# Kernel optimization log

Hardware: AMD Instinct MI355X
Metric: run time of the kernel (lower is better)

The kernel has to match this reference:

```python
import jax, jax.numpy as jnp
import numpy as np

DT = 0.1
TAU_MIN = 1.0
TAU_MAX = 10.0
LN_EPS = 1e-5


def setup_inputs() -> dict:
    key = jax.random.key(0)
    ks = jax.random.split(key, 8)
    B, S, I, H = 64, 1024, 256, 512
    s_in = 1.0 / np.sqrt(I)
    s_rec = 1.0 / np.sqrt(H)
    s_tau1 = 1.0 / np.sqrt(I + H)
    s_tau2 = 1.0 / np.sqrt(H)
    return {
        "x": jax.random.normal(ks[0], (B, S, I), dtype=jnp.float32),
        "h0": jnp.zeros((B, H), dtype=jnp.float32),
        "W_in": jax.random.uniform(ks[1], (H, I), jnp.float32, -s_in, s_in),
        "b_in": jax.random.uniform(ks[2], (H,), jnp.float32, -s_in, s_in),
        "W_rec": jax.random.uniform(ks[3], (H, H), jnp.float32, -s_rec, s_rec),
        "tau_w1": jax.random.uniform(ks[4], (H, I + H), jnp.float32, -s_tau1, s_tau1),
        "tau_b1": jax.random.uniform(ks[5], (H,), jnp.float32, -s_tau1, s_tau1),
        "tau_w2": jax.random.uniform(ks[6], (1, H), jnp.float32, -s_tau2, s_tau2),
        "tau_b2": jax.random.uniform(ks[7], (1,), jnp.float32, -s_tau2, s_tau2),
        "gamma": jnp.ones((H,), dtype=jnp.float32),
        "beta": jnp.zeros((H,), dtype=jnp.float32),
    }


def _layernorm(h, gamma, beta):
    mu = jnp.mean(h, axis=-1, keepdims=True)
    var = jnp.mean(jnp.square(h - mu), axis=-1, keepdims=True)
    return (h - mu) * jax.lax.rsqrt(var + LN_EPS) * gamma + beta


def reference(x, h0, W_in, b_in, W_rec, tau_w1, tau_b1, tau_w2, tau_b2, gamma, beta):
    # x: [B, S, I] -> scan over time with carry h: [B, H]
    def step(h, x_t):
        combined = jnp.concatenate([x_t, h], axis=-1)                     # [B, I+H]
        t_hid = jnp.tanh(combined @ tau_w1.T + tau_b1)                    # [B, H]
        tau_raw = jax.nn.sigmoid(t_hid @ tau_w2.T + tau_b2)               # [B, 1]
        tau = TAU_MIN + (TAU_MAX - TAU_MIN) * tau_raw                     # [B, 1]
        f_xh = jnp.tanh(x_t @ W_in.T + b_in + h @ W_rec.T)                # [B, H]
        h_new = h + DT * (-h + f_xh) / tau
        h_new = _layernorm(h_new, gamma, beta)
        return h_new, (h_new, tau)

    xs = jnp.swapaxes(x, 0, 1)                                            # [S, B, I]
    h_final, (outs, taus) = jax.lax.scan(step, h0, xs)
    output = jnp.swapaxes(outs, 0, 1)                                     # [B, S, H]
    tau_history = jnp.swapaxes(taus, 0, 1)                                # [B, S, 1]
    return output, h_final, tau_history
```

## Files before the change

### kernel.cpp

```cpp
#include <hip/hip_runtime.h>

#define S_LEN 1024
#define BATCH 64
#define I_DIM 256
#define H_DIM 512
#define NCL 8
#define NRK 8
#define ROWS 8
#define FPW 64
#define HSTR 520
#define XSTR 264
#define POLL_CAP 16384

typedef short short8 __attribute__((ext_vector_type(8)));
typedef float floatx4 __attribute__((ext_vector_type(4)));
typedef unsigned short ushortx4 __attribute__((ext_vector_type(4)));

__device__ inline unsigned short f2bf(float x){
  unsigned u = __float_as_uint(x);
  u += 0x7fffu + ((u >> 16) & 1u);
  return (unsigned short)(u >> 16);
}
__device__ inline float bf2f(unsigned short s){
  return __uint_as_float(((unsigned)s) << 16);
}
__device__ inline float fast_tanh(float x){
  float e = __expf(2.0f * x);
  return 1.0f - 2.0f / (e + 1.0f);
}
__device__ inline float fast_sigmoid(float x){
  return 1.0f / (1.0f + __expf(-x));
}
__device__ inline short8 cvt8(const float* p){
  short8 r;
#pragma unroll
  for (int j = 0; j < 8; j++) r[j] = (short)f2bf(p[j]);
  return r;
}

__global__ __launch_bounds__(256) void convert_weights_kernel(
  const float* __restrict__ W_in, const float* __restrict__ tau_w1,
  unsigned short* __restrict__ Wbf, unsigned short* __restrict__ Tbf)
{
  const int f = blockIdx.x, k = threadIdx.x;
  Wbf[f * I_DIM + k] = f2bf(W_in[(size_t)f * I_DIM + k]);
  Tbf[f * I_DIM + k] = f2bf(tau_w1[(size_t)f * (I_DIM + H_DIM) + k]);
}

__global__ __launch_bounds__(256) void precompute_kernel(
  const float* __restrict__ x, const unsigned short* __restrict__ Wbf,
  const unsigned short* __restrict__ Tbf,
  const float* __restrict__ b_in, const float* __restrict__ tau_b1,
  unsigned short* __restrict__ A_in, unsigned short* __restrict__ A_tau)
{
  __shared__ unsigned short xs[BATCH * XSTR];
  const int t = blockIdx.x, tid = threadIdx.x;
  {
    const int br = tid >> 2, pp = tid & 3;
    const float* xrow = x + ((size_t)br * S_LEN + t) * I_DIM + pp * 64;
    unsigned short* drow = xs + br * XSTR + pp * 64;
#pragma unroll
    for (int c = 0; c < 16; c++){
      float4 v = *(const float4*)(xrow + c * 4);
      ushortx4 o; o[0] = f2bf(v.x); o[1] = f2bf(v.y); o[2] = f2bf(v.z); o[3] = f2bf(v.w);
      *(ushortx4*)(drow + c * 4) = o;
    }
  }
  __syncthreads();

  const int w = tid >> 6, l15 = tid & 15, q = (tid & 63) >> 4;
#pragma unroll 1
  for (int fb = 0; fb < 8; fb++){
    const int F = fb * 64 + w * 16 + l15;
    floatx4 accf[4], acct[4];
#pragma unroll
    for (int m = 0; m < 4; m++){ accf[m] = (floatx4){0,0,0,0}; acct[m] = (floatx4){0,0,0,0}; }
#pragma unroll
    for (int kc = 0; kc < 8; kc++){
      const int k0 = kc * 32 + q * 8;
      short8 bw = *(const short8*)&Wbf[F * I_DIM + k0];
      short8 bt = *(const short8*)&Tbf[F * I_DIM + k0];
#pragma unroll
      for (int m = 0; m < 4; m++){
        short8 a = *(const short8*)&xs[(m * 16 + l15) * XSTR + k0];
        accf[m] = __builtin_amdgcn_mfma_f32_16x16x32_bf16(a, bw, accf[m], 0, 0, 0);
        acct[m] = __builtin_amdgcn_mfma_f32_16x16x32_bf16(a, bt, acct[m], 0, 0, 0);
      }
    }
    const float bi = b_in[F], bt1 = tau_b1[F];
#pragma unroll
    for (int m = 0; m < 4; m++){
      ushortx4 pf, pt;
#pragma unroll
      for (int i2 = 0; i2 < 4; i2++){ pf[i2] = f2bf(accf[m][i2] + bi); pt[i2] = f2bf(acct[m][i2] + bt1); }
      const size_t base = ((size_t)t * H_DIM + F) * BATCH + m * 16 + q * 4;
      *(ushortx4*)(A_in + base) = pf;
      *(ushortx4*)(A_tau + base) = pt;
    }
  }
}

__global__ __launch_bounds__(256, 1) void scan_kernel(
  const float* __restrict__ h0, const float* __restrict__ W_rec,
  const float* __restrict__ tau_w1, const float* __restrict__ tau_w2,
  const float* __restrict__ tau_b2_p, const float* __restrict__ gamma,
  const float* __restrict__ beta,
  const unsigned short* __restrict__ A_in, const unsigned short* __restrict__ A_tau,
  unsigned short* __restrict__ bc_f, float* __restrict__ bc_td,
  unsigned int* __restrict__ flags,
  float* __restrict__ out0, float* __restrict__ outh, float* __restrict__ outtau)
{
  __shared__ unsigned short hB[16 * HSTR];

  const int tid = threadIdx.x;
  const int cl   = blockIdx.x & (NCL - 1);
  const int rank = blockIdx.x >> 3;

  for (int idx = tid; idx < 16 * HSTR; idx += 256) hB[idx] = 0;

  const int w = tid >> 6, l64 = tid & 63, l15 = tid & 15, q = (tid & 63) >> 4;
  const int fl = l15;
  const int rb0 = (l64 >> 4) * 4;
  const bool pvalid = (l64 < 32);
  const int F0 = rank * FPW + w * 16;
  const int Fl = F0 + l15;
  const int rr = tid >> 5;
  const int cc = tid & 31;

  short8 wr[16], wt[16];
#pragma unroll
  for (int kc = 0; kc < 16; kc++){
    const int k = kc * 32 + q * 8;
    wr[kc] = cvt8(&W_rec[(size_t)Fl * H_DIM + k]);
    wt[kc] = cvt8(&tau_w1[(size_t)Fl * (I_DIM + H_DIM) + I_DIM + k]);
  }
  const float tw2v = tau_w2[Fl];
  const float tb2 = tau_b2_p[0];
  __syncthreads();

  float h_reg[16], gamr[16], betr[16];
  {
    const int b = cl * ROWS + rr;
#pragma unroll
    for (int j = 0; j < 16; j++){
      float hv = h0[(size_t)b * H_DIM + cc * 16 + j];
      h_reg[j] = hv;
      hB[rr * HSTR + cc * 16 + j] = f2bf(hv);
      gamr[j] = gamma[cc * 16 + j];
      betr[j] = beta[cc * 16 + j];
    }
  }

  ushortx4 afr = (ushortx4){0,0,0,0}, atr = (ushortx4){0,0,0,0};
  if (pvalid){
    const size_t aidx = ((size_t)Fl) * BATCH + cl * ROWS + rb0;
    afr = *(const ushortx4*)&A_in[aidx];
    atr = *(const ushortx4*)&A_tau[aidx];
  }
  __syncthreads();

  for (int t = 0; t < S_LEN; t++){
    const int par = t & 1;

    floatx4 af = {0,0,0,0}, at4 = {0,0,0,0};
#pragma unroll
    for (int kc = 0; kc < 16; kc++){
      short8 ha = *(const short8*)&hB[l15 * HSTR + kc * 32 + q * 8];
      af  = __builtin_amdgcn_mfma_f32_16x16x32_bf16(ha, wr[kc], af,  0, 0, 0);
      at4 = __builtin_amdgcn_mfma_f32_16x16x32_bf16(ha, wt[kc], at4, 0, 0, 0);
    }

    unsigned short* bcF = bc_f + ((size_t)(par * NCL + cl) * ROWS) * H_DIM;
    float pd[4];
#pragma unroll
    for (int i2 = 0; i2 < 4; i2++){
      float vf = fast_tanh(af[i2]  + bf2f(afr[i2]));
      float vt = fast_tanh(at4[i2] + bf2f(atr[i2]));
      pd[i2] = vt * tw2v;
      unsigned pv = (unsigned)f2bf(vf);
      unsigned ov = (unsigned)__shfl_xor((int)pv, 1);
      if (pvalid && !(fl & 1)){
        unsigned short* p = bcF + (size_t)(rb0 + i2) * H_DIM + F0 + fl;
        __hip_atomic_store((unsigned*)p, pv | (ov << 16),
                           __ATOMIC_RELAXED, __HIP_MEMORY_SCOPE_AGENT);
      }
    }
#pragma unroll
    for (int i2 = 0; i2 < 4; i2++){
      pd[i2] += __shfl_xor(pd[i2], 1);
      pd[i2] += __shfl_xor(pd[i2], 2);
      pd[i2] += __shfl_xor(pd[i2], 4);
      pd[i2] += __shfl_xor(pd[i2], 8);
    }
    if (pvalid && fl == 0){
      float* p = bc_td + ((size_t)(par * NCL + cl) * 32 + rank * 4 + w) * ROWS + rb0;
#pragma unroll
      for (int i2 = 0; i2 < 4; i2++)
        __hip_atomic_store(p + i2, pd[i2], __ATOMIC_RELAXED, __HIP_MEMORY_SCOPE_AGENT);
    }

    __builtin_amdgcn_s_waitcnt(0);
    __syncthreads();
    if (tid == 0)
      __hip_atomic_store(&flags[cl * NRK + rank], (unsigned)(t + 1),
                         __ATOMIC_RELAXED, __HIP_MEMORY_SCOPE_AGENT);
    if (t + 1 < S_LEN && pvalid){
      const size_t aidx = ((size_t)(t + 1) * H_DIM + Fl) * BATCH + cl * ROWS + rb0;
      afr = *(const ushortx4*)&A_in[aidx];
      atr = *(const ushortx4*)&A_tau[aidx];
    }
    if (w == 0 && l64 < NRK){
      const unsigned tgt = (unsigned)(t + 1);
      const unsigned int* fp = &flags[cl * NRK + l64];
      int guard = 0;
      while (__hip_atomic_load(fp, __ATOMIC_RELAXED, __HIP_MEMORY_SCOPE_AGENT) < tgt){
        if (++guard > POLL_CAP) break;
        __builtin_amdgcn_s_sleep(1);
      }
    }
    asm volatile("" ::: "memory");
    __syncthreads();

    const unsigned long long* p64 = (const unsigned long long*)
      (bc_f + (((size_t)(par * NCL + cl) * ROWS) + rr) * H_DIM + cc * 16);
    const float* tdp = bc_td + ((size_t)(par * NCL + cl) * 32 + cc) * ROWS + rr;
    unsigned long long v0 = __hip_atomic_load(p64 + 0, __ATOMIC_RELAXED, __HIP_MEMORY_SCOPE_AGENT);
    unsigned long long v1 = __hip_atomic_load(p64 + 1, __ATOMIC_RELAXED, __HIP_MEMORY_SCOPE_AGENT);
    unsigned long long v2 = __hip_atomic_load(p64 + 2, __ATOMIC_RELAXED, __HIP_MEMORY_SCOPE_AGENT);
    unsigned long long v3 = __hip_atomic_load(p64 + 3, __ATOMIC_RELAXED, __HIP_MEMORY_SCOPE_AGENT);
    float td = __hip_atomic_load(tdp, __ATOMIC_RELAXED, __HIP_MEMORY_SCOPE_AGENT);

    td += __shfl_xor(td, 1); td += __shfl_xor(td, 2);
    td += __shfl_xor(td, 4); td += __shfl_xor(td, 8);
    td += __shfl_xor(td, 16);
    const float tau = 1.0f + 9.0f * fast_sigmoid(td + tb2);
    const float c2 = 0.1f / tau, c1 = 1.0f - c2;

    float fv[16];
#pragma unroll
    for (int e = 0; e < 4; e++){
      fv[e]      = bf2f((unsigned short)(v0 >> (16 * e)));
      fv[4 + e]  = bf2f((unsigned short)(v1 >> (16 * e)));
      fv[8 + e]  = bf2f((unsigned short)(v2 >> (16 * e)));
      fv[12 + e] = bf2f((unsigned short)(v3 >> (16 * e)));
    }
    float hp[16]; float s1 = 0.f, s2 = 0.f;
#pragma unroll
    for (int j = 0; j < 16; j++){
      float v = c1 * h_reg[j] + c2 * fv[j];
      hp[j] = v; s1 += v; s2 += v * v;
    }
    s1 += __shfl_xor(s1, 1);  s2 += __shfl_xor(s2, 1);
    s1 += __shfl_xor(s1, 2);  s2 += __shfl_xor(s2, 2);
    s1 += __shfl_xor(s1, 4);  s2 += __shfl_xor(s2, 4);
    s1 += __shfl_xor(s1, 8);  s2 += __shfl_xor(s2, 8);
    s1 += __shfl_xor(s1, 16); s2 += __shfl_xor(s2, 16);
    const float mu = s1 * (1.0f / 512.0f);
    const float var = s2 * (1.0f / 512.0f) - mu * mu;
    const float rs = rsqrtf(var + 1e-5f);
#pragma unroll
    for (int j = 0; j < 16; j++) h_reg[j] = (hp[j] - mu) * rs * gamr[j] + betr[j];

#pragma unroll
    for (int u = 0; u < 2; u++){
      short8 hv;
#pragma unroll
      for (int e = 0; e < 8; e++) hv[e] = (short)f2bf(h_reg[u * 8 + e]);
      *(short8*)&hB[rr * HSTR + cc * 16 + u * 8] = hv;
    }

    if (rr == rank){
      float* dst = out0 + ((size_t)(cl * ROWS + rr) * S_LEN + t) * H_DIM + cc * 16;
#pragma unroll
      for (int j = 0; j < 16; j++) dst[j] = h_reg[j];
      if (cc == 0) outtau[(size_t)(cl * ROWS + rr) * S_LEN + t] = tau;
      if (t == S_LEN - 1){
        float* dh = outh + (size_t)(cl * ROWS + rr) * H_DIM + cc * 16;
#pragma unroll
        for (int j = 0; j < 16; j++) dh[j] = h_reg[j];
      }
    }
    __syncthreads();
  }
}

extern "C" void kernel_launch(void* const* d_in, const int* in_sizes, int n_in,
                              void* d_out, int out_size, void* d_ws, size_t ws_size,
                              hipStream_t stream) {
  const float* x      = (const float*)d_in[0];
  const float* h0     = (const float*)d_in[1];
  const float* W_in   = (const float*)d_in[2];
  const float* b_in   = (const float*)d_in[3];
  const float* W_rec  = (const float*)d_in[4];
  const float* tau_w1 = (const float*)d_in[5];
  const float* tau_b1 = (const float*)d_in[6];
  const float* tau_w2 = (const float*)d_in[7];
  const float* tau_b2 = (const float*)d_in[8];
  const float* gamma  = (const float*)d_in[9];
  const float* beta   = (const float*)d_in[10];

  char* ws = (char*)d_ws;
  unsigned short* A_in   = (unsigned short*)(ws);
  unsigned short* A_tau  = (unsigned short*)(ws + 67108864);
  unsigned short* bc_f   = (unsigned short*)(ws + 134217728);
  float*          bc_td  = (float*)(ws + 134348800);
  unsigned int*   flags  = (unsigned int*)(ws + 134365184);
  unsigned short* Wbf    = (unsigned short*)(ws + 134366208);
  unsigned short* Tbf    = (unsigned short*)(ws + 134628352);

  float* out0   = (float*)d_out;
  float* outh   = out0 + (size_t)BATCH * S_LEN * H_DIM;
  float* outtau = outh + (size_t)BATCH * H_DIM;

  hipMemsetAsync(flags, 0, 1024, stream);
  convert_weights_kernel<<<dim3(H_DIM), 256, 0, stream>>>(W_in, tau_w1, Wbf, Tbf);
  precompute_kernel<<<dim3(S_LEN), 256, 0, stream>>>(x, Wbf, Tbf, b_in, tau_b1, A_in, A_tau);
  scan_kernel<<<dim3(NCL * NRK), 256, 0, stream>>>(h0, W_rec, tau_w1, tau_w2, tau_b2, gamma, beta,
                                                   A_in, A_tau, bc_f, bc_td, flags,
                                                   out0, outh, outtau);
}
```

Baseline: 4.368 ms.

## Map each scan cluster to one XCD and use workgroup-scope atomics for exchange

At startup, each block reads its hardware XCD id and takes a slot in a per-XCD counter. This lets it join a cluster whose 8 ranks all sit on the same XCD. When every XCD holds a multiple of 8 blocks and a trial handshake succeeds, per-step communication uses workgroup-scope atomics, which are meant to stay in the local L2 and avoid device-coherent traffic. The flags are also padded to 64-byte spacing to avoid false sharing. This adds startup handshakes and falls back to agent scope otherwise, but relying on workgroup scope for cross-block visibility goes beyond what the memory model guarantees.

```diff
diff --git a/kernel.cpp b/kernel.cpp
--- a/kernel.cpp
+++ b/kernel.cpp
@@ -11,6 +11,8 @@
 #define HSTR 520
 #define XSTR 264
 #define POLL_CAP 16384
+#define HSHAKE_CAP 200000
+#define TRIAL_CAP 30000
 
 typedef short short8 __attribute__((ext_vector_type(8)));
 typedef float floatx4 __attribute__((ext_vector_type(4)));
@@ -36,6 +38,27 @@
 #pragma unroll
   for (int j = 0; j < 8; j++) r[j] = (short)f2bf(p[j]);
   return r;
+}
+
+__device__ inline void comm_st_u32(unsigned* p, unsigned v, bool fast){
+  if (fast) __hip_atomic_store(p, v, __ATOMIC_RELAXED, __HIP_MEMORY_SCOPE_WORKGROUP);
+  else      __hip_atomic_store(p, v, __ATOMIC_RELAXED, __HIP_MEMORY_SCOPE_AGENT);
+}
+__device__ inline void comm_st_f32(float* p, float v, bool fast){
+  if (fast) __hip_atomic_store(p, v, __ATOMIC_RELAXED, __HIP_MEMORY_SCOPE_WORKGROUP);
+  else      __hip_atomic_store(p, v, __ATOMIC_RELAXED, __HIP_MEMORY_SCOPE_AGENT);
+}
+__device__ inline unsigned comm_ld_u32(unsigned* p, bool fast){
+  if (fast) return __hip_atomic_fetch_add(p, 0u, __ATOMIC_RELAXED, __HIP_MEMORY_SCOPE_WORKGROUP);
+  else      return __hip_atomic_load(p, __ATOMIC_RELAXED, __HIP_MEMORY_SCOPE_AGENT);
+}
+__device__ inline unsigned long long comm_ld_u64(unsigned long long* p, bool fast){
+  if (fast) return __hip_atomic_fetch_add(p, 0ull, __ATOMIC_RELAXED, __HIP_MEMORY_SCOPE_WORKGROUP);
+  else      return __hip_atomic_load(p, __ATOMIC_RELAXED, __HIP_MEMORY_SCOPE_AGENT);
+}
+__device__ inline float comm_ld_f32(float* p, bool fast){
+  if (fast) return __hip_atomic_fetch_add(p, 0.0f, __ATOMIC_RELAXED, __HIP_MEMORY_SCOPE_WORKGROUP);
+  else      return __hip_atomic_load(p, __ATOMIC_RELAXED, __HIP_MEMORY_SCOPE_AGENT);
 }
 
 __global__ __launch_bounds__(256) void convert_weights_kernel(
@@ -111,12 +134,77 @@
   float* __restrict__ out0, float* __restrict__ outh, float* __restrict__ outtau)
 {
   __shared__ unsigned short hB[16 * HSTR];
+  __shared__ int sh_cl, sh_rk, sh_fast;
 
   const int tid = threadIdx.x;
-  const int cl   = blockIdx.x & (NCL - 1);
-  const int rank = blockIdx.x >> 3;
-
+
+  if (tid == 0){
+    unsigned xcd;
+    asm volatile("s_getreg_b32 %0, hwreg(HW_REG_XCC_ID)" : "=s"(xcd));
+    xcd &= 7u;
+    unsigned* initcnt = flags + 1024;
+    unsigned* g_cnt   = flags + 1040;
+    int slot = atomicAdd((int*)&initcnt[xcd], 1);
+    __builtin_amdgcn_s_waitcnt(0);
+    atomicAdd((int*)g_cnt, 1);
+    unsigned seen = 0; int hcap = 0;
+    for (;;){
+      seen = __hip_atomic_load(g_cnt, __ATOMIC_RELAXED, __HIP_MEMORY_SCOPE_AGENT);
+      if (seen >= 64u || ++hcap > HSHAKE_CAP) break;
+      __builtin_amdgcn_s_sleep(8);
+    }
+    int ok = (seen >= 64u) ? 1 : 0;
+    unsigned c8[8]; int pre = 0;
+#pragma unroll
+    for (int x2 = 0; x2 < 8; x2++){
+      c8[x2] = __hip_atomic_load(&initcnt[x2], __ATOMIC_RELAXED, __HIP_MEMORY_SCOPE_AGENT);
+      ok &= ((c8[x2] & 7u) == 0u);
+    }
+    for (unsigned y = 0; y < xcd; y++) pre += (int)(c8[y] >> 3);
+    if (ok){ sh_cl = pre + (slot >> 3); sh_rk = slot & 7; sh_fast = 1; }
+    else {
+      sh_cl = (int)(blockIdx.x & 7); sh_rk = (int)(blockIdx.x >> 3); sh_fast = 0;
+      __hip_atomic_store(&flags[1042], 1u, __ATOMIC_RELAXED, __HIP_MEMORY_SCOPE_AGENT);
+    }
+  }
   for (int idx = tid; idx < 16 * HSTR; idx += 256) hB[idx] = 0;
+  __syncthreads();
+  const int cl = sh_cl, rank = sh_rk;
+
+  if (sh_fast){
+    unsigned* T = flags + 1088;
+#pragma unroll 1
+    for (unsigned ph = 1; ph <= 2; ph++){
+      if (tid == 0) comm_st_u32(&T[(cl * 8 + rank) << 4], ph, true);
+      __builtin_amdgcn_s_waitcnt(0);
+      if (tid < 8){
+        int g = 0;
+        while (comm_ld_u32(&T[(cl * 8 + tid) << 4], true) < ph){
+          if (++g > TRIAL_CAP){
+            __hip_atomic_store(&flags[1042], 1u, __ATOMIC_RELAXED, __HIP_MEMORY_SCOPE_AGENT);
+            break;
+          }
+          __builtin_amdgcn_s_sleep(1);
+        }
+      }
+      __syncthreads();
+    }
+  }
+  if (tid == 0){
+    __builtin_amdgcn_s_waitcnt(0);
+    atomicAdd((int*)&flags[1041], 1);
+    unsigned seen2 = 0; int hcap2 = 0;
+    for (;;){
+      seen2 = __hip_atomic_load(&flags[1041], __ATOMIC_RELAXED, __HIP_MEMORY_SCOPE_AGENT);
+      if (seen2 >= 64u || ++hcap2 > HSHAKE_CAP) break;
+      __builtin_amdgcn_s_sleep(8);
+    }
+    unsigned dm = __hip_atomic_load(&flags[1042], __ATOMIC_RELAXED, __HIP_MEMORY_SCOPE_AGENT);
+    if (seen2 < 64u) dm = 1u;
+    if (dm) sh_fast = 0;
+  }
+  __syncthreads();
+  const bool fast = (sh_fast != 0);
 
   const int w = tid >> 6, l64 = tid & 63, l15 = tid & 15, q = (tid & 63) >> 4;
   const int fl = l15;
@@ -136,7 +224,6 @@
   }
   const float tw2v = tau_w2[Fl];
   const float tb2 = tau_b2_p[0];
-  __syncthreads();
 
   float h_reg[16], gamr[16], betr[16];
   {
@@ -181,8 +268,7 @@
       unsigned ov = (unsigned)__shfl_xor((int)pv, 1);
       if (pvalid && !(fl & 1)){
         unsigned short* p = bcF + (size_t)(rb0 + i2) * H_DIM + F0 + fl;
-        __hip_atomic_store((unsigned*)p, pv | (ov << 16),
-                           __ATOMIC_RELAXED, __HIP_MEMORY_SCOPE_AGENT);
+        comm_st_u32((unsigned*)p, pv | (ov << 16), fast);
       }
     }
 #pragma unroll
@@ -195,15 +281,13 @@
     if (pvalid && fl == 0){
       float* p = bc_td + ((size_t)(par * NCL + cl) * 32 + rank * 4 + w) * ROWS + rb0;
 #pragma unroll
-      for (int i2 = 0; i2 < 4; i2++)
-        __hip_atomic_store(p + i2, pd[i2], __ATOMIC_RELAXED, __HIP_MEMORY_SCOPE_AGENT);
+      for (int i2 = 0; i2 < 4; i2++) comm_st_f32(p + i2, pd[i2], fast);
     }
 
     __builtin_amdgcn_s_waitcnt(0);
     __syncthreads();
     if (tid == 0)
-      __hip_atomic_store(&flags[cl * NRK + rank], (unsigned)(t + 1),
-                         __ATOMIC_RELAXED, __HIP_MEMORY_SCOPE_AGENT);
+      comm_st_u32(&flags[(cl * NRK + rank) << 4], (unsigned)(t + 1), fast);
     if (t + 1 < S_LEN && pvalid){
       const size_t aidx = ((size_t)(t + 1) * H_DIM + Fl) * BATCH + cl * ROWS + rb0;
       afr = *(const ushortx4*)&A_in[aidx];
@@ -211,9 +295,9 @@
     }
     if (w == 0 && l64 < NRK){
       const unsigned tgt = (unsigned)(t + 1);
-      const unsigned int* fp = &flags[cl * NRK + l64];
+      unsigned* fp = &flags[(cl * NRK + l64) << 4];
       int guard = 0;
-      while (__hip_atomic_load(fp, __ATOMIC_RELAXED, __HIP_MEMORY_SCOPE_AGENT) < tgt){
+      while (comm_ld_u32(fp, fast) < tgt){
         if (++guard > POLL_CAP) break;
         __builtin_amdgcn_s_sleep(1);
       }
@@ -221,14 +305,14 @@
     asm volatile("" ::: "memory");
     __syncthreads();
 
-    const unsigned long long* p64 = (const unsigned long long*)
+    unsigned long long* p64 = (unsigned long long*)
       (bc_f + (((size_t)(par * NCL + cl) * ROWS) + rr) * H_DIM + cc * 16);
-    const float* tdp = bc_td + ((size_t)(par * NCL + cl) * 32 + cc) * ROWS + rr;
-    unsigned long long v0 = __hip_atomic_load(p64 + 0, __ATOMIC_RELAXED, __HIP_MEMORY_SCOPE_AGENT);
-    unsigned long long v1 = __hip_atomic_load(p64 + 1, __ATOMIC_RELAXED, __HIP_MEMORY_SCOPE_AGENT);
-    unsigned long long v2 = __hip_atomic_load(p64 + 2, __ATOMIC_RELAXED, __HIP_MEMORY_SCOPE_AGENT);
-    unsigned long long v3 = __hip_atomic_load(p64 + 3, __ATOMIC_RELAXED, __HIP_MEMORY_SCOPE_AGENT);
-    float td = __hip_atomic_load(tdp, __ATOMIC_RELAXED, __HIP_MEMORY_SCOPE_AGENT);
+    float* tdp = bc_td + ((size_t)(par * NCL + cl) * 32 + cc) * ROWS + rr;
+    unsigned long long v0 = comm_ld_u64(p64 + 0, fast);
+    unsigned long long v1 = comm_ld_u64(p64 + 1, fast);
+    unsigned long long v2 = comm_ld_u64(p64 + 2, fast);
+    unsigned long long v3 = comm_ld_u64(p64 + 3, fast);
+    float td = comm_ld_f32(tdp, fast);
 
     td += __shfl_xor(td, 1); td += __shfl_xor(td, 2);
     td += __shfl_xor(td, 4); td += __shfl_xor(td, 8);
@@ -305,14 +389,14 @@
   unsigned short* bc_f   = (unsigned short*)(ws + 134217728);
   float*          bc_td  = (float*)(ws + 134348800);
   unsigned int*   flags  = (unsigned int*)(ws + 134365184);
-  unsigned short* Wbf    = (unsigned short*)(ws + 134366208);
-  unsigned short* Tbf    = (unsigned short*)(ws + 134628352);
+  unsigned short* Wbf    = (unsigned short*)(ws + 134381568);
+  unsigned short* Tbf    = (unsigned short*)(ws + 134643712);
 
   float* out0   = (float*)d_out;
   float* outh   = out0 + (size_t)BATCH * S_LEN * H_DIM;
   float* outtau = outh + (size_t)BATCH * H_DIM;
 
-  hipMemsetAsync(flags, 0, 1024, stream);
+  hipMemsetAsync(flags, 0, 16384, stream);
   convert_weights_kernel<<<dim3(H_DIM), 256, 0, stream>>>(W_in, tau_w1, Wbf, Tbf);
   precompute_kernel<<<dim3(S_LEN), 256, 0, stream>>>(x, Wbf, Tbf, b_in, tau_b1, A_in, A_tau);
   scan_kernel<<<dim3(NCL * NRK), 256, 0, stream>>>(h0, W_rec, tau_w1, tau_w2, tau_b2, gamma, beta,
```

New measurement: 6.722 ms. 53.9% more time.

## Split each cluster's batch rows into two 4-row groups and pad flags

Applied to the files above, without the earlier changes.

Each block now processes two independent 4-row batch groups (A and B). Each group runs its own MFMA chain and broadcast buffers. The post-barrier LayerNorm is remapped to one wave per row, with 8 features per lane. Per-block progress flags are spaced 64 bytes apart to avoid false sharing during polling. This trades a doubled per-step MFMA count, since each 16-row tile now holds only 4 valid rows, for different broadcast and flag-contention behaviour.

```diff
diff --git a/kernel.cpp b/kernel.cpp
--- a/kernel.cpp
+++ b/kernel.cpp
@@ -4,13 +4,12 @@
 #define BATCH 64
 #define I_DIM 256
 #define H_DIM 512
-#define NCL 8
+#define NCLP 8
 #define NRK 8
-#define ROWS 8
-#define FPW 64
+#define RPC 4
 #define HSTR 520
 #define XSTR 264
-#define POLL_CAP 16384
+#define POLL_CAP 20000
 
 typedef short short8 __attribute__((ext_vector_type(8)));
 typedef float floatx4 __attribute__((ext_vector_type(4)));
@@ -36,6 +35,21 @@
 #pragma unroll
   for (int j = 0; j < 8; j++) r[j] = (short)f2bf(p[j]);
   return r;
+}
+__device__ inline void ast_u32(unsigned* p, unsigned v){
+  __hip_atomic_store(p, v, __ATOMIC_RELAXED, __HIP_MEMORY_SCOPE_AGENT);
+}
+__device__ inline void ast_f32(float* p, float v){
+  __hip_atomic_store(p, v, __ATOMIC_RELAXED, __HIP_MEMORY_SCOPE_AGENT);
+}
+__device__ inline unsigned ald_u32(const unsigned* p){
+  return __hip_atomic_load(p, __ATOMIC_RELAXED, __HIP_MEMORY_SCOPE_AGENT);
+}
+__device__ inline unsigned long long ald_u64(const unsigned long long* p){
+  return __hip_atomic_load(p, __ATOMIC_RELAXED, __HIP_MEMORY_SCOPE_AGENT);
+}
+__device__ inline float ald_f32(const float* p){
+  return __hip_atomic_load(p, __ATOMIC_RELAXED, __HIP_MEMORY_SCOPE_AGENT);
 }
 
 __global__ __launch_bounds__(256) void convert_weights_kernel(
@@ -110,22 +124,21 @@
   unsigned int* __restrict__ flags,
   float* __restrict__ out0, float* __restrict__ outh, float* __restrict__ outtau)
 {
-  __shared__ unsigned short hB[16 * HSTR];
+  __shared__ unsigned short hA[16 * HSTR];
+  __shared__ unsigned short hBs[16 * HSTR];
 
   const int tid = threadIdx.x;
-  const int cl   = blockIdx.x & (NCL - 1);
+  const int c    = blockIdx.x & 7;
   const int rank = blockIdx.x >> 3;
-
-  for (int idx = tid; idx < 16 * HSTR; idx += 256) hB[idx] = 0;
-
-  const int w = tid >> 6, l64 = tid & 63, l15 = tid & 15, q = (tid & 63) >> 4;
+  const int w = tid >> 6, l64 = tid & 63, l15 = l64 & 15, q = l64 >> 4;
   const int fl = l15;
-  const int rb0 = (l64 >> 4) * 4;
-  const bool pvalid = (l64 < 32);
-  const int F0 = rank * FPW + w * 16;
+  const bool pvalid = (l64 < 16);
+  const int F0 = rank * 64 + w * 16;
   const int Fl = F0 + l15;
-  const int rr = tid >> 5;
-  const int cc = tid & 31;
+  const int rr = w;
+  const int lane = l64;
+
+  for (int idx = tid; idx < 16 * HSTR; idx += 256){ hA[idx] = 0; hBs[idx] = 0; }
 
   short8 wr[16], wt[16];
 #pragma unroll
@@ -138,82 +151,112 @@
   const float tb2 = tau_b2_p[0];
   __syncthreads();
 
-  float h_reg[16], gamr[16], betr[16];
-  {
-    const int b = cl * ROWS + rr;
-#pragma unroll
-    for (int j = 0; j < 16; j++){
-      float hv = h0[(size_t)b * H_DIM + cc * 16 + j];
-      h_reg[j] = hv;
-      hB[rr * HSTR + cc * 16 + j] = f2bf(hv);
-      gamr[j] = gamma[cc * 16 + j];
-      betr[j] = beta[cc * 16 + j];
-    }
-  }
-
-  ushortx4 afr = (ushortx4){0,0,0,0}, atr = (ushortx4){0,0,0,0};
+  const int bA = c * RPC + rr;
+  const int bB = 32 + c * RPC + rr;
+  float h_A[8], h_B[8], gamr[8], betr[8];
+#pragma unroll
+  for (int j = 0; j < 8; j++){
+    float va = h0[(size_t)bA * H_DIM + lane * 8 + j];
+    float vb = h0[(size_t)bB * H_DIM + lane * 8 + j];
+    h_A[j] = va; h_B[j] = vb;
+    hA [rr * HSTR + lane * 8 + j] = f2bf(va);
+    hBs[rr * HSTR + lane * 8 + j] = f2bf(vb);
+    gamr[j] = gamma[lane * 8 + j];
+    betr[j] = beta[lane * 8 + j];
+  }
+
+  ushortx4 afA = (ushortx4){0,0,0,0}, atA = afA, afB = afA, atB = afA;
   if (pvalid){
-    const size_t aidx = ((size_t)Fl) * BATCH + cl * ROWS + rb0;
-    afr = *(const ushortx4*)&A_in[aidx];
-    atr = *(const ushortx4*)&A_tau[aidx];
+    const size_t ai = ((size_t)Fl) * BATCH;
+    afA = *(const ushortx4*)&A_in [ai + c * RPC];
+    atA = *(const ushortx4*)&A_tau[ai + c * RPC];
+    afB = *(const ushortx4*)&A_in [ai + 32 + c * RPC];
+    atB = *(const ushortx4*)&A_tau[ai + 32 + c * RPC];
   }
   __syncthreads();
 
   for (int t = 0; t < S_LEN; t++){
     const int par = t & 1;
 
-    floatx4 af = {0,0,0,0}, at4 = {0,0,0,0};
-#pragma unroll
-    for (int kc = 0; kc < 16; kc++){
-      short8 ha = *(const short8*)&hB[l15 * HSTR + kc * 32 + q * 8];
-      af  = __builtin_amdgcn_mfma_f32_16x16x32_bf16(ha, wr[kc], af,  0, 0, 0);
-      at4 = __builtin_amdgcn_mfma_f32_16x16x32_bf16(ha, wt[kc], at4, 0, 0, 0);
-    }
-
-    unsigned short* bcF = bc_f + ((size_t)(par * NCL + cl) * ROWS) * H_DIM;
-    float pd[4];
-#pragma unroll
-    for (int i2 = 0; i2 < 4; i2++){
-      float vf = fast_tanh(af[i2]  + bf2f(afr[i2]));
-      float vt = fast_tanh(at4[i2] + bf2f(atr[i2]));
-      pd[i2] = vt * tw2v;
-      unsigned pv = (unsigned)f2bf(vf);
-      unsigned ov = (unsigned)__shfl_xor((int)pv, 1);
-      if (pvalid && !(fl & 1)){
-        unsigned short* p = bcF + (size_t)(rb0 + i2) * H_DIM + F0 + fl;
-        __hip_atomic_store((unsigned*)p, pv | (ov << 16),
-                           __ATOMIC_RELAXED, __HIP_MEMORY_SCOPE_AGENT);
-      }
-    }
-#pragma unroll
-    for (int i2 = 0; i2 < 4; i2++){
-      pd[i2] += __shfl_xor(pd[i2], 1);
-      pd[i2] += __shfl_xor(pd[i2], 2);
-      pd[i2] += __shfl_xor(pd[i2], 4);
-      pd[i2] += __shfl_xor(pd[i2], 8);
-    }
-    if (pvalid && fl == 0){
-      float* p = bc_td + ((size_t)(par * NCL + cl) * 32 + rank * 4 + w) * ROWS + rb0;
-#pragma unroll
-      for (int i2 = 0; i2 < 4; i2++)
-        __hip_atomic_store(p + i2, pd[i2], __ATOMIC_RELAXED, __HIP_MEMORY_SCOPE_AGENT);
+    {
+      floatx4 af = {0,0,0,0}, at4 = {0,0,0,0};
+#pragma unroll
+      for (int kc = 0; kc < 16; kc++){
+        short8 ha = *(const short8*)&hA[l15 * HSTR + kc * 32 + q * 8];
+        af  = __builtin_amdgcn_mfma_f32_16x16x32_bf16(ha, wr[kc], af,  0, 0, 0);
+        at4 = __builtin_amdgcn_mfma_f32_16x16x32_bf16(ha, wt[kc], at4, 0, 0, 0);
+      }
+      unsigned short* bcF = bc_f + ((size_t)(par * 16 + c) * RPC) * H_DIM;
+      float pd[4];
+#pragma unroll
+      for (int i2 = 0; i2 < 4; i2++){
+        float vf = fast_tanh(af[i2]  + bf2f(afA[i2]));
+        float vt = fast_tanh(at4[i2] + bf2f(atA[i2]));
+        pd[i2] = vt * tw2v;
+        unsigned pv = (unsigned)f2bf(vf);
+        unsigned ov = (unsigned)__shfl_xor((int)pv, 1);
+        if (pvalid && !(fl & 1))
+          ast_u32((unsigned*)(bcF + (size_t)i2 * H_DIM + F0 + fl), pv | (ov << 16));
+      }
+#pragma unroll
+      for (int i2 = 0; i2 < 4; i2++){
+        pd[i2] += __shfl_xor(pd[i2], 1); pd[i2] += __shfl_xor(pd[i2], 2);
+        pd[i2] += __shfl_xor(pd[i2], 4); pd[i2] += __shfl_xor(pd[i2], 8);
+      }
+      if (pvalid && fl == 0){
+        float* p = bc_td + ((size_t)(par * 16 + c) * 32 + rank * 4 + w) * RPC;
+#pragma unroll
+        for (int i2 = 0; i2 < 4; i2++) ast_f32(p + i2, pd[i2]);
+      }
+    }
+    {
+      floatx4 af = {0,0,0,0}, at4 = {0,0,0,0};
+#pragma unroll
+      for (int kc = 0; kc < 16; kc++){
+        short8 ha = *(const short8*)&hBs[l15 * HSTR + kc * 32 + q * 8];
+        af  = __builtin_amdgcn_mfma_f32_16x16x32_bf16(ha, wr[kc], af,  0, 0, 0);
+        at4 = __builtin_amdgcn_mfma_f32_16x16x32_bf16(ha, wt[kc], at4, 0, 0, 0);
+      }
+      unsigned short* bcF = bc_f + ((size_t)(par * 16 + c + 8) * RPC) * H_DIM;
+      float pd[4];
+#pragma unroll
+      for (int i2 = 0; i2 < 4; i2++){
+        float vf = fast_tanh(af[i2]  + bf2f(afB[i2]));
+        float vt = fast_tanh(at4[i2] + bf2f(atB[i2]));
+        pd[i2] = vt * tw2v;
+        unsigned pv = (unsigned)f2bf(vf);
+        unsigned ov = (unsigned)__shfl_xor((int)pv, 1);
+        if (pvalid && !(fl & 1))
+          ast_u32((unsigned*)(bcF + (size_t)i2 * H_DIM + F0 + fl), pv | (ov << 16));
+      }
+#pragma unroll
+      for (int i2 = 0; i2 < 4; i2++){
+        pd[i2] += __shfl_xor(pd[i2], 1); pd[i2] += __shfl_xor(pd[i2], 2);
+        pd[i2] += __shfl_xor(pd[i2], 4); pd[i2] += __shfl_xor(pd[i2], 8);
+      }
+      if (pvalid && fl == 0){
+        float* p = bc_td + ((size_t)(par * 16 + c + 8) * 32 + rank * 4 + w) * RPC;
+#pragma unroll
+        for (int i2 = 0; i2 < 4; i2++) ast_f32(p + i2, pd[i2]);
+      }
     }
 
     __builtin_amdgcn_s_waitcnt(0);
     __syncthreads();
     if (tid == 0)
-      __hip_atomic_store(&flags[cl * NRK + rank], (unsigned)(t + 1),
-                         __ATOMIC_RELAXED, __HIP_MEMORY_SCOPE_AGENT);
+      ast_u32(&flags[(c * 8 + rank) << 4], (unsigned)(t + 1));
     if (t + 1 < S_LEN && pvalid){
-      const size_t aidx = ((size_t)(t + 1) * H_DIM + Fl) * BATCH + cl * ROWS + rb0;
-      afr = *(const ushortx4*)&A_in[aidx];
-      atr = *(const ushortx4*)&A_tau[aidx];
+      const size_t ai = ((size_t)(t + 1) * H_DIM + Fl) * BATCH;
+      afA = *(const ushortx4*)&A_in [ai + c * RPC];
+      atA = *(const ushortx4*)&A_tau[ai + c * RPC];
+      afB = *(const ushortx4*)&A_in [ai + 32 + c * RPC];
+      atB = *(const ushortx4*)&A_tau[ai + 32 + c * RPC];
     }
     if (w == 0 && l64 < NRK){
       const unsigned tgt = (unsigned)(t + 1);
-      const unsigned int* fp = &flags[cl * NRK + l64];
+      const unsigned* fp = &flags[(c * 8 + l64) << 4];
       int guard = 0;
-      while (__hip_atomic_load(fp, __ATOMIC_RELAXED, __HIP_MEMORY_SCOPE_AGENT) < tgt){
+      while (ald_u32(fp) < tgt){
         if (++guard > POLL_CAP) break;
         __builtin_amdgcn_s_sleep(1);
       }
@@ -221,63 +264,109 @@
     asm volatile("" ::: "memory");
     __syncthreads();
 
-    const unsigned long long* p64 = (const unsigned long long*)
-      (bc_f + (((size_t)(par * NCL + cl) * ROWS) + rr) * H_DIM + cc * 16);
-    const float* tdp = bc_td + ((size_t)(par * NCL + cl) * 32 + cc) * ROWS + rr;
-    unsigned long long v0 = __hip_atomic_load(p64 + 0, __ATOMIC_RELAXED, __HIP_MEMORY_SCOPE_AGENT);
-    unsigned long long v1 = __hip_atomic_load(p64 + 1, __ATOMIC_RELAXED, __HIP_MEMORY_SCOPE_AGENT);
-    unsigned long long v2 = __hip_atomic_load(p64 + 2, __ATOMIC_RELAXED, __HIP_MEMORY_SCOPE_AGENT);
-    unsigned long long v3 = __hip_atomic_load(p64 + 3, __ATOMIC_RELAXED, __HIP_MEMORY_SCOPE_AGENT);
-    float td = __hip_atomic_load(tdp, __ATOMIC_RELAXED, __HIP_MEMORY_SCOPE_AGENT);
-
-    td += __shfl_xor(td, 1); td += __shfl_xor(td, 2);
-    td += __shfl_xor(td, 4); td += __shfl_xor(td, 8);
-    td += __shfl_xor(td, 16);
-    const float tau = 1.0f + 9.0f * fast_sigmoid(td + tb2);
-    const float c2 = 0.1f / tau, c1 = 1.0f - c2;
-
-    float fv[16];
-#pragma unroll
-    for (int e = 0; e < 4; e++){
-      fv[e]      = bf2f((unsigned short)(v0 >> (16 * e)));
-      fv[4 + e]  = bf2f((unsigned short)(v1 >> (16 * e)));
-      fv[8 + e]  = bf2f((unsigned short)(v2 >> (16 * e)));
-      fv[12 + e] = bf2f((unsigned short)(v3 >> (16 * e)));
-    }
-    float hp[16]; float s1 = 0.f, s2 = 0.f;
-#pragma unroll
-    for (int j = 0; j < 16; j++){
-      float v = c1 * h_reg[j] + c2 * fv[j];
-      hp[j] = v; s1 += v; s2 += v * v;
-    }
-    s1 += __shfl_xor(s1, 1);  s2 += __shfl_xor(s2, 1);
-    s1 += __shfl_xor(s1, 2);  s2 += __shfl_xor(s2, 2);
-    s1 += __shfl_xor(s1, 4);  s2 += __shfl_xor(s2, 4);
-    s1 += __shfl_xor(s1, 8);  s2 += __shfl_xor(s2, 8);
-    s1 += __shfl_xor(s1, 16); s2 += __shfl_xor(s2, 16);
-    const float mu = s1 * (1.0f / 512.0f);
-    const float var = s2 * (1.0f / 512.0f) - mu * mu;
-    const float rs = rsqrtf(var + 1e-5f);
-#pragma unroll
-    for (int j = 0; j < 16; j++) h_reg[j] = (hp[j] - mu) * rs * gamr[j] + betr[j];
-
-#pragma unroll
-    for (int u = 0; u < 2; u++){
+    const unsigned long long* pA = (const unsigned long long*)
+      (bc_f + (((size_t)(par * 16 + c) * RPC) + rr) * H_DIM + lane * 8);
+    const unsigned long long* pB = (const unsigned long long*)
+      (bc_f + (((size_t)(par * 16 + c + 8) * RPC) + rr) * H_DIM + lane * 8);
+    unsigned long long a0 = ald_u64(pA + 0);
+    unsigned long long a1 = ald_u64(pA + 1);
+    unsigned long long b0 = ald_u64(pB + 0);
+    unsigned long long b1 = ald_u64(pB + 1);
+    float tdA = ald_f32(bc_td + ((size_t)(par * 16 + c)     * 32 + (lane & 31)) * RPC + rr);
+    float tdB = ald_f32(bc_td + ((size_t)(par * 16 + c + 8) * 32 + (lane & 31)) * RPC + rr);
+
+    {
+      float td = tdA;
+      td += __shfl_xor(td, 1); td += __shfl_xor(td, 2);
+      td += __shfl_xor(td, 4); td += __shfl_xor(td, 8);
+      td += __shfl_xor(td, 16);
+      const float tau = 1.0f + 9.0f * fast_sigmoid(td + tb2);
+      const float c2 = 0.1f / tau, c1 = 1.0f - c2;
+      float fv[8];
+#pragma unroll
+      for (int e = 0; e < 4; e++){
+        fv[e]     = bf2f((unsigned short)(a0 >> (16 * e)));
+        fv[4 + e] = bf2f((unsigned short)(a1 >> (16 * e)));
+      }
+      float hp[8]; float s1 = 0.f, s2 = 0.f;
+#pragma unroll
+      for (int j = 0; j < 8; j++){
+        float v = c1 * h_A[j] + c2 * fv[j];
+        hp[j] = v; s1 += v; s2 += v * v;
+      }
+      s1 += __shfl_xor(s1, 1);  s2 += __shfl_xor(s2, 1);
+      s1 += __shfl_xor(s1, 2);  s2 += __shfl_xor(s2, 2);
+      s1 += __shfl_xor(s1, 4);  s2 += __shfl_xor(s2, 4);
+      s1 += __shfl_xor(s1, 8);  s2 += __shfl_xor(s2, 8);
+      s1 += __shfl_xor(s1, 16); s2 += __shfl_xor(s2, 16);
+      s1 += __shfl_xor(s1, 32); s2 += __shfl_xor(s2, 32);
+      const float mu = s1 * (1.0f / 512.0f);
+      const float var = s2 * (1.0f / 512.0f) - mu * mu;
+      const float rs = rsqrtf(var + 1e-5f);
       short8 hv;
 #pragma unroll
-      for (int e = 0; e < 8; e++) hv[e] = (short)f2bf(h_reg[u * 8 + e]);
-      *(short8*)&hB[rr * HSTR + cc * 16 + u * 8] = hv;
-    }
-
-    if (rr == rank){
-      float* dst = out0 + ((size_t)(cl * ROWS + rr) * S_LEN + t) * H_DIM + cc * 16;
-#pragma unroll
-      for (int j = 0; j < 16; j++) dst[j] = h_reg[j];
-      if (cc == 0) outtau[(size_t)(cl * ROWS + rr) * S_LEN + t] = tau;
-      if (t == S_LEN - 1){
-        float* dh = outh + (size_t)(cl * ROWS + rr) * H_DIM + cc * 16;
-#pragma unroll
-        for (int j = 0; j < 16; j++) dh[j] = h_reg[j];
+      for (int j = 0; j < 8; j++){
+        h_A[j] = (hp[j] - mu) * rs * gamr[j] + betr[j];
+        hv[j] = (short)f2bf(h_A[j]);
+      }
+      *(short8*)&hA[rr * HSTR + lane * 8] = hv;
+      if ((lane >> 3) == rank){
+        float* dst = out0 + ((size_t)bA * S_LEN + t) * H_DIM + lane * 8;
+#pragma unroll
+        for (int j = 0; j < 8; j++) dst[j] = h_A[j];
+      }
+      if (rank == 0 && lane == 0) outtau[(size_t)bA * S_LEN + t] = tau;
+      if (t == S_LEN - 1 && rank == 0){
+        float* dh = outh + (size_t)bA * H_DIM + lane * 8;
+#pragma unroll
+        for (int j = 0; j < 8; j++) dh[j] = h_A[j];
+      }
+    }
+    {
+      float td = tdB;
+      td += __shfl_xor(td, 1); td += __shfl_xor(td, 2);
+      td += __shfl_xor(td, 4); td += __shfl_xor(td, 8);
+      td += __shfl_xor(td, 16);
+      const float tau = 1.0f + 9.0f * fast_sigmoid(td + tb2);
+      const float c2 = 0.1f / tau, c1 = 1.0f - c2;
+      float fv[8];
+#pragma unroll
+      for (int e = 0; e < 4; e++){
+        fv[e]     = bf2f((unsigned short)(b0 >> (16 * e)));
+        fv[4 + e] = bf2f((unsigned short)(b1 >> (16 * e)));
+      }
+      float hp[8]; float s1 = 0.f, s2 = 0.f;
+#pragma unroll
+      for (int j = 0; j < 8; j++){
+        float v = c1 * h_B[j] + c2 * fv[j];
+        hp[j] = v; s1 += v; s2 += v * v;
+      }
+      s1 += __shfl_xor(s1, 1);  s2 += __shfl_xor(s2, 1);
+      s1 += __shfl_xor(s1, 2);  s2 += __shfl_xor(s2, 2);
+      s1 += __shfl_xor(s1, 4);  s2 += __shfl_xor(s2, 4);
+      s1 += __shfl_xor(s1, 8);  s2 += __shfl_xor(s2, 8);
+      s1 += __shfl_xor(s1, 16); s2 += __shfl_xor(s2, 16);
+      s1 += __shfl_xor(s1, 32); s2 += __shfl_xor(s2, 32);
+      const float mu = s1 * (1.0f / 512.0f);
+      const float var = s2 * (1.0f / 512.0f) - mu * mu;
+      const float rs = rsqrtf(var + 1e-5f);
+      short8 hv;
+#pragma unroll
+      for (int j = 0; j < 8; j++){
+        h_B[j] = (hp[j] - mu) * rs * gamr[j] + betr[j];
+        hv[j] = (short)f2bf(h_B[j]);
+      }
+      *(short8*)&hBs[rr * HSTR + lane * 8] = hv;
+      if ((lane >> 3) == rank){
+        float* dst = out0 + ((size_t)bB * S_LEN + t) * H_DIM + lane * 8;
+#pragma unroll
+        for (int j = 0; j < 8; j++) dst[j] = h_B[j];
+      }
+      if (rank == 0 && lane == 0) outtau[(size_t)bB * S_LEN + t] = tau;
+      if (t == S_LEN - 1 && rank == 0){
+        float* dh = outh + (size_t)bB * H_DIM + lane * 8;
+#pragma unroll
+        for (int j = 0; j < 8; j++) dh[j] = h_B[j];
       }
     }
     __syncthreads();
@@ -305,17 +394,17 @@
   unsigned short* bc_f   = (unsigned short*)(ws + 134217728);
   float*          bc_td  = (float*)(ws + 134348800);
   unsigned int*   flags  = (unsigned int*)(ws + 134365184);
-  unsigned short* Wbf    = (unsigned short*)(ws + 134366208);
-  unsigned short* Tbf    = (unsigned short*)(ws + 134628352);
+  unsigned short* Wbf    = (unsigned short*)(ws + 134381568);
+  unsigned short* Tbf    = (unsigned short*)(ws + 134643712);
 
   float* out0   = (float*)d_out;
   float* outh   = out0 + (size_t)BATCH * S_LEN * H_DIM;
   float* outtau = outh + (size_t)BATCH * H_DIM;
 
-  hipMemsetAsync(flags, 0, 1024, stream);
+  hipMemsetAsync(flags, 0, 16384, stream);
   convert_weights_kernel<<<dim3(H_DIM), 256, 0, stream>>>(W_in, tau_w1, Wbf, Tbf);
   precompute_kernel<<<dim3(S_LEN), 256, 0, stream>>>(x, Wbf, Tbf, b_in, tau_b1, A_in, A_tau);
-  scan_kernel<<<dim3(NCL * NRK), 256, 0, stream>>>(h0, W_rec, tau_w1, tau_w2, tau_b2, gamma, beta,
-                                                   A_in, A_tau, bc_f, bc_td, flags,
-                                                   out0, outh, outtau);
-}
+  scan_kernel<<<dim3(NCLP * NRK), 256, 0, stream>>>(h0, W_rec, tau_w1, tau_w2, tau_b2, gamma, beta,
+                                                    A_in, A_tau, bc_f, bc_td, flags,
+                                                    out0, outh, outtau);
+}
```

Result: slower. 6.661 ms (+52.5%).

## Replace per-block flag barrier with tagged tau partials as per-thread sync tokens

Applied to the files above, without the earlier changes.

Removes the separate per-cluster flag array and the barrier-plus-flag-store handshake. Each tau partial is now stored as a 64-bit word carrying the step number in its upper half, and every consumer thread spins on its own tagged word instead of one wave polling flags behind a block barrier. This removes one __syncthreads and a serialized flag round trip per timestep. The catch is that correctness depends on the f data stores being visible before the tag store: the code waits on its own stores before issuing the tag, but other lanes' f stores are not ordered by that wait. All 256 threads now poll global memory, which adds memory traffic.

```diff
diff --git a/kernel.cpp b/kernel.cpp
--- a/kernel.cpp
+++ b/kernel.cpp
@@ -10,7 +10,7 @@
 #define FPW 64
 #define HSTR 520
 #define XSTR 264
-#define POLL_CAP 16384
+#define POLL_CAP 20000
 
 typedef short short8 __attribute__((ext_vector_type(8)));
 typedef float floatx4 __attribute__((ext_vector_type(4)));
@@ -36,6 +36,15 @@
 #pragma unroll
   for (int j = 0; j < 8; j++) r[j] = (short)f2bf(p[j]);
   return r;
+}
+__device__ inline void ast_u32(unsigned* p, unsigned v){
+  __hip_atomic_store(p, v, __ATOMIC_RELAXED, __HIP_MEMORY_SCOPE_AGENT);
+}
+__device__ inline void ast_u64(unsigned long long* p, unsigned long long v){
+  __hip_atomic_store(p, v, __ATOMIC_RELAXED, __HIP_MEMORY_SCOPE_AGENT);
+}
+__device__ inline unsigned long long ald_u64(const unsigned long long* p){
+  return __hip_atomic_load(p, __ATOMIC_RELAXED, __HIP_MEMORY_SCOPE_AGENT);
 }
 
 __global__ __launch_bounds__(256) void convert_weights_kernel(
@@ -106,8 +115,7 @@
   const float* __restrict__ tau_b2_p, const float* __restrict__ gamma,
   const float* __restrict__ beta,
   const unsigned short* __restrict__ A_in, const unsigned short* __restrict__ A_tau,
-  unsigned short* __restrict__ bc_f, float* __restrict__ bc_td,
-  unsigned int* __restrict__ flags,
+  unsigned short* __restrict__ bc_f, unsigned long long* __restrict__ bc_tag,
   float* __restrict__ out0, float* __restrict__ outh, float* __restrict__ outtau)
 {
   __shared__ unsigned short hB[16 * HSTR];
@@ -181,8 +189,7 @@
       unsigned ov = (unsigned)__shfl_xor((int)pv, 1);
       if (pvalid && !(fl & 1)){
         unsigned short* p = bcF + (size_t)(rb0 + i2) * H_DIM + F0 + fl;
-        __hip_atomic_store((unsigned*)p, pv | (ov << 16),
-                           __ATOMIC_RELAXED, __HIP_MEMORY_SCOPE_AGENT);
+        ast_u32((unsigned*)p, pv | (ov << 16));
       }
     }
 #pragma unroll
@@ -192,43 +199,42 @@
       pd[i2] += __shfl_xor(pd[i2], 4);
       pd[i2] += __shfl_xor(pd[i2], 8);
     }
+
+    __builtin_amdgcn_s_waitcnt(0);
+    asm volatile("" ::: "memory");
     if (pvalid && fl == 0){
-      float* p = bc_td + ((size_t)(par * NCL + cl) * 32 + rank * 4 + w) * ROWS + rb0;
+      unsigned long long* tp =
+        bc_tag + (((size_t)(par * NCL + cl)) * 32 + rank * 4 + w) * 8 + rb0;
+      const unsigned long long tag = ((unsigned long long)(t + 1)) << 32;
 #pragma unroll
       for (int i2 = 0; i2 < 4; i2++)
-        __hip_atomic_store(p + i2, pd[i2], __ATOMIC_RELAXED, __HIP_MEMORY_SCOPE_AGENT);
-    }
-
-    __builtin_amdgcn_s_waitcnt(0);
-    __syncthreads();
-    if (tid == 0)
-      __hip_atomic_store(&flags[cl * NRK + rank], (unsigned)(t + 1),
-                         __ATOMIC_RELAXED, __HIP_MEMORY_SCOPE_AGENT);
+        ast_u64(tp + i2, tag | (unsigned long long)__float_as_uint(pd[i2]));
+    }
     if (t + 1 < S_LEN && pvalid){
       const size_t aidx = ((size_t)(t + 1) * H_DIM + Fl) * BATCH + cl * ROWS + rb0;
       afr = *(const ushortx4*)&A_in[aidx];
       atr = *(const ushortx4*)&A_tau[aidx];
     }
-    if (w == 0 && l64 < NRK){
-      const unsigned tgt = (unsigned)(t + 1);
-      const unsigned int* fp = &flags[cl * NRK + l64];
-      int guard = 0;
-      while (__hip_atomic_load(fp, __ATOMIC_RELAXED, __HIP_MEMORY_SCOPE_AGENT) < tgt){
-        if (++guard > POLL_CAP) break;
-        __builtin_amdgcn_s_sleep(1);
-      }
+    __syncthreads();
+
+    const unsigned long long* tp =
+      bc_tag + (((size_t)(par * NCL + cl)) * 32 + cc) * 8 + rr;
+    unsigned long long tv; int guard = 0;
+    const unsigned tgt = (unsigned)(t + 1);
+    for (;;){
+      tv = ald_u64(tp);
+      if ((unsigned)(tv >> 32) >= tgt || ++guard > POLL_CAP) break;
+      __builtin_amdgcn_s_sleep(1);
     }
     asm volatile("" ::: "memory");
-    __syncthreads();
+    float td = __uint_as_float((unsigned)tv);
 
     const unsigned long long* p64 = (const unsigned long long*)
       (bc_f + (((size_t)(par * NCL + cl) * ROWS) + rr) * H_DIM + cc * 16);
-    const float* tdp = bc_td + ((size_t)(par * NCL + cl) * 32 + cc) * ROWS + rr;
-    unsigned long long v0 = __hip_atomic_load(p64 + 0, __ATOMIC_RELAXED, __HIP_MEMORY_SCOPE_AGENT);
-    unsigned long long v1 = __hip_atomic_load(p64 + 1, __ATOMIC_RELAXED, __HIP_MEMORY_SCOPE_AGENT);
-    unsigned long long v2 = __hip_atomic_load(p64 + 2, __ATOMIC_RELAXED, __HIP_MEMORY_SCOPE_AGENT);
-    unsigned long long v3 = __hip_atomic_load(p64 + 3, __ATOMIC_RELAXED, __HIP_MEMORY_SCOPE_AGENT);
-    float td = __hip_atomic_load(tdp, __ATOMIC_RELAXED, __HIP_MEMORY_SCOPE_AGENT);
+    unsigned long long v0 = ald_u64(p64 + 0);
+    unsigned long long v1 = ald_u64(p64 + 1);
+    unsigned long long v2 = ald_u64(p64 + 2);
+    unsigned long long v3 = ald_u64(p64 + 3);
 
     td += __shfl_xor(td, 1); td += __shfl_xor(td, 2);
     td += __shfl_xor(td, 4); td += __shfl_xor(td, 8);
@@ -300,22 +306,21 @@
   const float* beta   = (const float*)d_in[10];
 
   char* ws = (char*)d_ws;
-  unsigned short* A_in   = (unsigned short*)(ws);
-  unsigned short* A_tau  = (unsigned short*)(ws + 67108864);
-  unsigned short* bc_f   = (unsigned short*)(ws + 134217728);
-  float*          bc_td  = (float*)(ws + 134348800);
-  unsigned int*   flags  = (unsigned int*)(ws + 134365184);
-  unsigned short* Wbf    = (unsigned short*)(ws + 134366208);
-  unsigned short* Tbf    = (unsigned short*)(ws + 134628352);
+  unsigned short*     A_in   = (unsigned short*)(ws);
+  unsigned short*     A_tau  = (unsigned short*)(ws + 67108864);
+  unsigned short*     bc_f   = (unsigned short*)(ws + 134217728);
+  unsigned long long* bc_tag = (unsigned long long*)(ws + 134348800);
+  unsigned short*     Wbf    = (unsigned short*)(ws + 134381568);
+  unsigned short*     Tbf    = (unsigned short*)(ws + 134643712);
 
   float* out0   = (float*)d_out;
   float* outh   = out0 + (size_t)BATCH * S_LEN * H_DIM;
   float* outtau = outh + (size_t)BATCH * H_DIM;
 
-  hipMemsetAsync(flags, 0, 1024, stream);
+  hipMemsetAsync(bc_tag, 0, 32768, stream);
   convert_weights_kernel<<<dim3(H_DIM), 256, 0, stream>>>(W_in, tau_w1, Wbf, Tbf);
   precompute_kernel<<<dim3(S_LEN), 256, 0, stream>>>(x, Wbf, Tbf, b_in, tau_b1, A_in, A_tau);
   scan_kernel<<<dim3(NCL * NRK), 256, 0, stream>>>(h0, W_rec, tau_w1, tau_w2, tau_b2, gamma, beta,
-                                                   A_in, A_tau, bc_f, bc_td, flags,
+                                                   A_in, A_tau, bc_f, bc_tag,
                                                    out0, outh, outtau);
 }
```

New measurement: 3.649 ms. 16.5% less time.
